# Optimization experiments

Measured on AMD Instinct MI355X. Metric: run time of the kernel, lower is better.

## Reference

```python
import jax, jax.numpy as jnp
import numpy as np

H = 768        # hidden_size (rubert-base)
WDIM = 30      # width_embedding_dim (SpanRepresentation default)
MAXW = 10      # max_span_width
HID = 150      # PairwiseScorer hidden_dim
LN_EPS = 1e-5


def setup_inputs() -> dict:
    key = jax.random.key(0)
    ks = jax.random.split(key, 12)
    B, S, N = 4, 2048, 4096
    p = lambda i, shape: jax.random.normal(ks[i], shape, dtype=jnp.float32) * 0.02
    return {
        "sequence_output": jax.random.normal(ks[0], (B, S, H), dtype=jnp.float32),
        "span_starts": jax.random.randint(ks[1], (B, N), 0, S),
        "span_ends": jax.random.randint(ks[2], (B, N), 0, S),
        "W_start": p(3, (H, H)), "b_start": jnp.zeros((H,), jnp.float32),
        "W_end": p(4, (H, H)), "b_end": jnp.zeros((H,), jnp.float32),
        "width_emb": p(5, (MAXW + 1, WDIM)),
        "W_out": p(6, (2 * H + WDIM, H)), "b_out": jnp.zeros((H,), jnp.float32),
        "w_ment": p(7, (H,)), "b_ment": jnp.zeros((), jnp.float32),
        "W1": p(8, (4 * H, HID)), "b1": jnp.zeros((HID,), jnp.float32),
        "ln_g": jnp.ones((HID,), jnp.float32), "ln_b": jnp.zeros((HID,), jnp.float32),
        "W2": p(9, (HID,)), "b2": jnp.zeros((), jnp.float32),
        "top_k": 128,
    }


def reference(sequence_output, span_starts, span_ends,
              W_start, b_start, W_end, b_end, width_emb, W_out, b_out,
              w_ment, b_ment, W1, b1, ln_g, ln_b, W2, b2, top_k):
    # --- SpanRepresentation: gather endpoints, endpoint FFs, width embedding ---
    st = jnp.take_along_axis(sequence_output, span_starts[..., None], axis=1)  # [B,N,H]
    en = jnp.take_along_axis(sequence_output, span_ends[..., None], axis=1)    # [B,N,H]
    start_e = st @ W_start + b_start
    end_e = en @ W_end + b_end
    widths = jnp.clip(span_ends - span_starts, 0, MAXW)
    we = width_emb[widths]                                                     # [B,N,WDIM]
    span_repr = jnp.concatenate([start_e, end_e, we], axis=-1) @ W_out + b_out # [B,N,H]

    # --- MentionScorer + top-k filtering (per batch, vectorized) ---
    scores = span_repr @ w_ment + b_ment                                       # [B,N]
    mention_scores, idx = jax.lax.top_k(scores, top_k)                         # [B,K]
    repr_k = jnp.take_along_axis(span_repr, idx[..., None], axis=1)            # [B,K,H]
    f_starts = jnp.take_along_axis(span_starts, idx, axis=1)
    f_ends = jnp.take_along_axis(span_ends, idx, axis=1)

    # --- PairwiseScorer over all pairs: cat([s1,s2,s1-s2,s1*s2]) @ W1 ---
    # Split W1 rows into the four feature blocks; fold the (s1-s2) block in:
    #   z = s1@(Wa+Wc) + s2@(Wb-Wc) + (s1*s2)@Wd + b1
    Wa, Wb, Wc, Wd = W1[:H], W1[H:2*H], W1[2*H:3*H], W1[3*H:]
    u = repr_k @ (Wa + Wc)                                                     # [B,K,HID]
    v = repr_k @ (Wb - Wc)                                                     # [B,K,HID]
    pw = jnp.einsum('bih,bjh,hd->bijd', repr_k, repr_k, Wd)                    # [B,K,K,HID]
    z = u[:, :, None, :] + v[:, None, :, :] + pw + b1
    h = jax.nn.relu(z)
    mu = jnp.mean(h, axis=-1, keepdims=True)
    var = jnp.mean(jnp.square(h - mu), axis=-1, keepdims=True)
    hn = (h - mu) * jax.lax.rsqrt(var + LN_EPS) * ln_g + ln_b
    # Dropout(0.3) is identity in eval mode.
    ant = hn @ W2 + b2                                                         # [B,K,K]
    ant = jnp.tril(ant, k=-1)

    return (mention_scores, ant, f_starts, f_ends)
```

## Files before the change

### kernel.cpp

```cpp
#include <hip/hip_runtime.h>
#include <math.h>

#define H 768
#define SEQ 2048
#define NSP 4096
#define HIDD 150
#define TOPK 128
#define NPAD 160

#define OFS_ANT 512
#define OFS_FS 66048
#define OFS_FE 66560

static const size_t OFF_T     = 0ull;
static const size_t OFF_BIASP = 8448ull;
static const size_t OFF_WOV   = 14592ull;
static const size_t OFF_AV    = 16128ull;
static const size_t OFF_CV    = 16896ull;
static const size_t OFF_TW    = 17664ull;
static const size_t OFF_PD    = 17680ull;
static const size_t OFF_CAND  = 34064ull;
static const size_t OFF_FS    = 42256ull;
static const size_t OFF_FE    = 42768ull;
static const size_t OFF_WID   = 43280ull;
static const size_t OFF_UVP   = 43792ull;
static const size_t OFF_GW    = 371472ull;
static const size_t OFF_SCAL  = 371632ull;
static const size_t OFF_WF    = 371640ull;
static const size_t OFF_WCF   = 433080ull;
static const size_t OFF_WSF   = 555960ull;
static const size_t OFF_WEF   = 850872ull;
static const size_t OFF_WOF   = 1145784ull;
static const size_t OFF_SEH   = 1735608ull;
static const size_t OFF_RKH   = 2128824ull;

typedef __attribute__((ext_vector_type(8))) _Float16 half8;
typedef __attribute__((ext_vector_type(4))) _Float16 half4;
typedef __attribute__((ext_vector_type(4))) float f32x4;

__global__ __launch_bounds__(256) void kA(
    const float* __restrict__ b_start, const float* __restrict__ b_end,
    const float* __restrict__ b_out, const float* __restrict__ W_out,
    const float* __restrict__ w_ment, const float* __restrict__ W1,
    const float* __restrict__ ln_g, const float* __restrict__ ln_b,
    const float* __restrict__ W2, const float* __restrict__ b2,
    const float* __restrict__ W_start, const float* __restrict__ W_end,
    float* __restrict__ biasP, float* __restrict__ WOV,
    _Float16* __restrict__ WF, _Float16* __restrict__ WCF,
    _Float16* __restrict__ WSF, _Float16* __restrict__ WEF,
    _Float16* __restrict__ WOF, float* __restrict__ GW, float* __restrict__ SCAL,
    float* __restrict__ ant) {
    const int blk = blockIdx.x, tid = threadIdx.x;
    if (blk < 24) {
        const int kc = blk / 3, jb = blk - kc * 3;
        const int j = jb * 256 + tid;
        float acc = (kc == 0) ? b_out[j] : 0.f;
        const int k0 = kc * 96;
#pragma unroll 4
        for (int k = k0; k < k0 + 96; ++k) {
            acc += b_start[k] * W_out[(size_t)k * H + j];
            acc += b_end[k]   * W_out[(size_t)(H + k) * H + j];
        }
        biasP[kc * H + j] = acc;
    } else if (blk < 408) {
        const int wid = tid >> 6, lane = tid & 63;
        const int gr = (blk - 24) * 4 + wid;
        const float* row = W_out + (size_t)gr * H;
        float s = 0.f;
#pragma unroll
        for (int q = 0; q < 12; ++q) s += row[lane + 64 * q] * w_ment[lane + 64 * q];
#pragma unroll
        for (int off = 32; off; off >>= 1) s += __shfl_down(s, off, 64);
        if (lane == 0) WOV[gr] = s;
    } else if (blk < 468) {
        const int idx = (blk - 408) * 256 + tid;
        const int nt = idx / 1536;
        const int rem = idx - nt * 1536;
        const int kt = rem >> 6, lane = rem & 63;
        const int n = nt * 16 + (lane & 15);
        const int kb = kt * 32 + (lane >> 4) * 8;
        _Float16* dst = WF + ((size_t)((kt * 10 + nt) * 64 + lane)) * 8;
#pragma unroll
        for (int e = 0; e < 8; ++e) {
            float v = (n < HIDD) ? W1[(size_t)(3 * H + kb + e) * HIDD + n] : 0.f;
            dst[e] = (_Float16)v;
        }
    } else if (blk < 588) {
        const int idx = (blk - 468) * 256 + tid;
        const int nt = idx / 1536;
        const int rem = idx - nt * 1536;
        const int kt = rem >> 6, lane = rem & 63;
        const int n = nt * 16 + (lane & 15);
        const int kb = kt * 32 + (lane >> 4) * 8;
        _Float16* dst = WCF + (size_t)idx * 8;
#pragma unroll
        for (int e = 0; e < 8; ++e) {
            const int h = kb + e;
            float v = 0.f;
            if (n < 160) {
                if (n < HIDD)
                    v = W1[(size_t)h * HIDD + n] + W1[(size_t)(2 * H + h) * HIDD + n];
            } else {
                const int d = n - 160;
                if (d < HIDD)
                    v = W1[(size_t)(H + h) * HIDD + d] - W1[(size_t)(2 * H + h) * HIDD + d];
            }
            dst[e] = (_Float16)v;
        }
    } else if (blk == 588) {
        if (tid < NPAD) GW[tid] = (tid < HIDD) ? ln_g[tid] * W2[tid] : 0.f;
        if (tid == 0) {
            float sg = 0.f, sb = 0.f;
            for (int d = 0; d < HIDD; ++d) { sg += ln_g[d] * W2[d]; sb += ln_b[d] * W2[d]; }
            SCAL[0] = sg;
            SCAL[1] = sb + b2[0];
        }
    } else if (blk < 1165) {
        const bool isS = blk < 877;
        const int idx = (blk - (isS ? 589 : 877)) * 256 + tid;
        const float* Wsrc = isS ? W_start : W_end;
        _Float16* dstb = isS ? WSF : WEF;
        const int nt = idx / 1536;
        const int rem = idx - nt * 1536;
        const int kt = rem >> 6, lane = rem & 63;
        const int n = nt * 16 + (lane & 15);
        const int kb = kt * 32 + (lane >> 4) * 8;
        _Float16* dst = dstb + (size_t)idx * 8;
#pragma unroll
        for (int e = 0; e < 8; ++e) dst[e] = (_Float16)Wsrc[(size_t)(kb + e) * H + n];
    } else if (blk < 1741) {
        const int idx = (blk - 1165) * 256 + tid;
        const int nt = idx / 3072;
        const int rem = idx - nt * 3072;
        const int kt = rem >> 6, lane = rem & 63;
        const int n = nt * 16 + (lane & 15);
        const int kb = kt * 32 + (lane >> 4) * 8;
        _Float16* dst = WOF + (size_t)idx * 8;
#pragma unroll
        for (int e = 0; e < 8; ++e) dst[e] = (_Float16)W_out[(size_t)(kb + e) * H + n];
    } else {
        const int idx = (blk - 1741) * 256 + tid;
        *(float4*)(ant + (size_t)idx * 4) = make_float4(0.f, 0.f, 0.f, 0.f);
    }
}

__global__ __launch_bounds__(256) void kB(
    const float* __restrict__ biasP, const float* __restrict__ width_emb,
    const float* __restrict__ W_out, const float* __restrict__ W_start,
    const float* __restrict__ W_end, const float* __restrict__ WOV,
    float* __restrict__ T, float* __restrict__ av, float* __restrict__ cv) {
    const int blk = blockIdx.x, tid = threadIdx.x;
    if (blk < 33) {
        const int w = blk / 3, jb = blk - w * 3;
        const int j = jb * 256 + tid;
        float acc = 0.f;
#pragma unroll
        for (int kc = 0; kc < 8; ++kc) acc += biasP[kc * H + j];
#pragma unroll
        for (int k = 0; k < 30; ++k)
            acc += width_emb[w * 30 + k] * W_out[(size_t)(2 * H + k) * H + j];
        T[w * H + j] = acc;
    } else {
        const int wid = tid >> 6, lane = tid & 63;
        const int gr = (blk - 33) * 4 + wid;
        const float* row = (gr < H) ? (W_start + (size_t)gr * H) : (W_end + (size_t)(gr - H) * H);
        const float* vec = (gr < H) ? WOV : (WOV + H);
        float s = 0.f;
#pragma unroll
        for (int q = 0; q < 12; ++q) s += row[lane + 64 * q] * vec[lane + 64 * q];
#pragma unroll
        for (int off = 32; off; off >>= 1) s += __shfl_down(s, off, 64);
        if (lane == 0) {
            if (gr < H) av[gr] = s; else cv[gr - H] = s;
        }
    }
}

__global__ void k_posdots(const float* __restrict__ seq, const float* __restrict__ av,
                          const float* __restrict__ cv, const float* __restrict__ T,
                          const float* __restrict__ w_ment, const float* __restrict__ b_ment,
                          float* __restrict__ PD, float* __restrict__ tw) {
    const int wid = threadIdx.x >> 6, lane = threadIdx.x & 63;
    if (blockIdx.x < 2048) {
        const int r = blockIdx.x * 4 + wid;
        const float4* row = (const float4*)(seq + (size_t)r * H);
        const float4* a4 = (const float4*)av;
        const float4* c4 = (const float4*)cv;
        float sa = 0.f, sc = 0.f;
#pragma unroll
        for (int q = 0; q < 3; ++q) {
            float4 x = row[lane + 64 * q];
            float4 ya = a4[lane + 64 * q], yc = c4[lane + 64 * q];
            sa += x.x * ya.x + x.y * ya.y + x.z * ya.z + x.w * ya.w;
            sc += x.x * yc.x + x.y * yc.y + x.z * yc.z + x.w * yc.w;
        }
#pragma unroll
        for (int off = 32; off; off >>= 1) {
            sa += __shfl_down(sa, off, 64);
            sc += __shfl_down(sc, off, 64);
        }
        if (lane == 0) { PD[r] = sa; PD[8192 + r] = sc; }
    } else {
        for (int w = wid; w <= 10; w += 4) {
            float s = 0.f;
#pragma unroll
            for (int q = 0; q < 12; ++q) s += T[w * H + lane + 64 * q] * w_ment[lane + 64 * q];
#pragma unroll
            for (int off = 32; off; off >>= 1) s += __shfl_down(s, off, 64);
            if (lane == 0) tw[w] = s + b_ment[0];
        }
    }
}

__global__ __launch_bounds__(256) void k_sort1(const float* __restrict__ PD,
    const int* __restrict__ starts, const int* __restrict__ ends,
    const float* __restrict__ tw, unsigned long long* __restrict__ CAND) {
    __shared__ unsigned long long keys[512];
    const int blk = blockIdx.x;
    const int b = blk >> 3, c = blk & 7;
    const int tid = threadIdx.x;
    for (int i = tid; i < 512; i += 256) {
        const int gi = c * 512 + i;
        const int r = b * NSP + gi;
        const int s = starts[r], e = ends[r];
        int w = e - s; w = w < 0 ? 0 : (w > 10 ? 10 : w);
        const float sc = PD[b * SEQ + s] + PD[8192 + b * SEQ + e] + tw[w];
        unsigned u = __float_as_uint(sc);
        u = (u & 0x80000000u) ? ~u : (u | 0x80000000u);
        keys[i] = ((unsigned long long)u << 32) | (unsigned)(0xFFFFFFFFu - (unsigned)gi);
    }
    __syncthreads();
    for (int k = 2; k <= 512; k <<= 1) {
        for (int j = k >> 1; j > 0; j >>= 1) {
            const int p = tid;
            const int i = ((p & ~(j - 1)) << 1) | (p & (j - 1));
            const int l = i | j;
            unsigned long long a = keys[i], d = keys[l];
            const bool desc = ((i & k) == 0);
            if ((a < d) == desc) { keys[i] = d; keys[l] = a; }
            __syncthreads();
        }
    }
    if (tid < 128) CAND[(size_t)(b * 8 + c) * 128 + tid] = keys[tid];
}

__global__ __launch_bounds__(256) void k_sort2(const unsigned long long* __restrict__ CAND,
    const int* __restrict__ starts, const int* __restrict__ ends,
    float* __restrict__ out, int* __restrict__ fsI, int* __restrict__ feI,
    int* __restrict__ widI) {
    __shared__ unsigned long long K[1024];
    const int b = blockIdx.x, tid = threadIdx.x;
    for (int i = tid; i < 1024; i += 256) K[i] = CAND[(size_t)b * 1024 + i];
    __syncthreads();
    for (int nl = 4; nl >= 1; nl >>= 1) {
        const int items = nl * 128;
        unsigned long long v0 = 0, v1 = 0;
        if (tid < items) {
            const int q = tid >> 7, r = tid & 127;
            unsigned long long a = K[q * 256 + r];
            unsigned long long d = K[q * 256 + 128 + (127 - r)];
            v0 = a > d ? a : d;
        }
        if (tid + 256 < items) {
            const int i = tid + 256;
            const int q = i >> 7, r = i & 127;
            unsigned long long a = K[q * 256 + r];
            unsigned long long d = K[q * 256 + 128 + (127 - r)];
            v1 = a > d ? a : d;
        }
        __syncthreads();
        if (tid < items) K[(tid >> 7) * 128 + (tid & 127)] = v0;
        if (tid + 256 < items) { const int i = tid + 256; K[(i >> 7) * 128 + (i & 127)] = v1; }
        __syncthreads();
        for (int j = 64; j; j >>= 1) {
            const int pairs = nl * 64;
            for (int i = tid; i < pairs; i += 256) {
                const int q = i >> 6, r = i & 63;
                const int lo = q * 128 + (((r & ~(j - 1)) << 1) | (r & (j - 1)));
                const int hi = lo + j;
                unsigned long long a = K[lo], d = K[hi];
                if (a < d) { K[lo] = d; K[hi] = a; }
            }
            __syncthreads();
        }
    }
    if (tid < TOPK) {
        const unsigned long long key = K[tid];
        const int widx = (int)(0xFFFFFFFFu - (unsigned)(key & 0xFFFFFFFFu));
        const unsigned hu = (unsigned)(key >> 32);
        const float sval = __uint_as_float((hu & 0x80000000u) ? (hu & 0x7FFFFFFFu) : ~hu);
        const int s = starts[b * NSP + widx], e = ends[b * NSP + widx];
        const int p = b * TOPK + tid;
        out[p] = sval;
        out[OFS_FS + p] = (float)s;
        out[OFS_FE + p] = (float)e;
        fsI[p] = b * SEQ + s;
        feI[p] = b * SEQ + e;
        int w = e - s;
        widI[p] = w < 0 ? 0 : (w > 10 ? 10 : w);
    }
}

__global__ __launch_bounds__(256) void k_gemm1(const float* __restrict__ seq,
    const int* __restrict__ fsI, const int* __restrict__ feI,
    const _Float16* __restrict__ WSF, const _Float16* __restrict__ WEF,
    _Float16* __restrict__ SEH) {
    const int mt = blockIdx.x;
    const int wave = threadIdx.x >> 6, lane = threadIdx.x & 63;
    const int g = lane >> 4;
    const int nt0 = blockIdx.y * 8 + wave * 2;
    const int gi = mt * 16 + (lane & 15);
    const int src = (mt < 32) ? fsI[gi] : feI[gi - 512];
    const float* Arow = seq + (size_t)src * H + g * 8;
    const _Float16* BF = (mt < 32) ? WSF : WEF;
    f32x4 acc0 = {0.f, 0.f, 0.f, 0.f}, acc1 = acc0;
    for (int kt = 0; kt < 24; ++kt) {
        float4 v0 = *(const float4*)(Arow + kt * 32);
        float4 v1 = *(const float4*)(Arow + kt * 32 + 4);
        half8 a = {(_Float16)v0.x, (_Float16)v0.y, (_Float16)v0.z, (_Float16)v0.w,
                   (_Float16)v1.x, (_Float16)v1.y, (_Float16)v1.z, (_Float16)v1.w};
        half8 b0 = *(const half8*)(BF + ((size_t)((nt0 * 24 + kt) * 64 + lane)) * 8);
        half8 b1 = *(const half8*)(BF + ((size_t)(((nt0 + 1) * 24 + kt) * 64 + lane)) * 8);
        acc0 = __builtin_amdgcn_mfma_f32_16x16x32_f16(a, b0, acc0, 0, 0, 0);
        acc1 = __builtin_amdgcn_mfma_f32_16x16x32_f16(a, b1, acc1, 0, 0, 0);
    }
    const int c = lane & 15, quad = lane >> 4;
#pragma unroll
    for (int r = 0; r < 4; ++r) {
        const int row = mt * 16 + quad * 4 + r;
        SEH[(size_t)row * H + nt0 * 16 + c] = (_Float16)acc0[r];
        SEH[(size_t)row * H + (nt0 + 1) * 16 + c] = (_Float16)acc1[r];
    }
}

__global__ __launch_bounds__(256) void k_gemm2(const _Float16* __restrict__ SEH,
    const _Float16* __restrict__ WOF, const float* __restrict__ T,
    const int* __restrict__ widI, _Float16* __restrict__ RKH) {
    const int mt = blockIdx.x;
    const int wave = threadIdx.x >> 6, lane = threadIdx.x & 63;
    const int nt0 = blockIdx.y * 8 + wave * 2;
    const _Float16* A0 = SEH + (size_t)(mt * 16 + (lane & 15)) * H + (lane >> 4) * 8;
    const _Float16* A1 = SEH + (size_t)(512 + mt * 16 + (lane & 15)) * H + (lane >> 4) * 8;
    f32x4 acc0 = {0.f, 0.f, 0.f, 0.f}, acc1 = acc0;
    for (int kt = 0; kt < 48; ++kt) {
        half8 a = (kt < 24) ? *(const half8*)(A0 + kt * 32)
                            : *(const half8*)(A1 + (kt - 24) * 32);
        half8 b0 = *(const half8*)(WOF + ((size_t)((nt0 * 48 + kt) * 64 + lane)) * 8);
        half8 b1 = *(const half8*)(WOF + ((size_t)(((nt0 + 1) * 48 + kt) * 64 + lane)) * 8);
        acc0 = __builtin_amdgcn_mfma_f32_16x16x32_f16(a, b0, acc0, 0, 0, 0);
        acc1 = __builtin_amdgcn_mfma_f32_16x16x32_f16(a, b1, acc1, 0, 0, 0);
    }
    const int c = lane & 15, quad = lane >> 4;
#pragma unroll
    for (int r = 0; r < 4; ++r) {
        const int row = mt * 16 + quad * 4 + r;
        const float* Tr = T + (size_t)widI[row] * H;
        RKH[(size_t)row * H + nt0 * 16 + c] = (_Float16)(acc0[r] + Tr[nt0 * 16 + c]);
        RKH[(size_t)row * H + (nt0 + 1) * 16 + c] = (_Float16)(acc1[r] + Tr[(nt0 + 1) * 16 + c]);
    }
}

__global__ __launch_bounds__(256) void k_uv3(const _Float16* __restrict__ RKH,
    const _Float16* __restrict__ WCF, float* __restrict__ UVP) {
    const int t = blockIdx.x, kh = blockIdx.y;
    const int wave = threadIdx.x >> 6, lane = threadIdx.x & 63;
    const _Float16* Arow = RKH + (size_t)(t * 16 + (lane & 15)) * H + (lane >> 4) * 8;
    f32x4 acc[5];
#pragma unroll
    for (int q = 0; q < 5; ++q) acc[q] = (f32x4){0.f, 0.f, 0.f, 0.f};
    for (int kk = 0; kk < 12; ++kk) {
        const int kt = kh * 12 + kk;
        half8 a = *(const half8*)(Arow + kt * 32);
#pragma unroll
        for (int q = 0; q < 5; ++q) {
            const int nt = wave * 5 + q;
            half8 bv = *(const half8*)(WCF + ((size_t)((nt * 24 + kt) * 64 + lane)) * 8);
            acc[q] = __builtin_amdgcn_mfma_f32_16x16x32_f16(a, bv, acc[q], 0, 0, 0);
        }
    }
    const int c = lane & 15, g = lane >> 4;
#pragma unroll
    for (int q = 0; q < 5; ++q) {
        const int n = (wave * 5 + q) * 16 + c;
#pragma unroll
        for (int r = 0; r < 4; ++r) {
            const int p = t * 16 + g * 4 + r;
            UVP[((size_t)kh * 512 + p) * 320 + n] = acc[q][r];
        }
    }
}

__global__ __launch_bounds__(256) void k_pair(
    const _Float16* __restrict__ WF, const _Float16* __restrict__ RKH,
    const float* __restrict__ UVP, const float* __restrict__ b1,
    const float* __restrict__ GW, const float* __restrict__ SCAL,
    float* __restrict__ ant) {
    const int b = blockIdx.y;
    int ti = 0, rem = blockIdx.x;
    while (rem >= (ti >> 1) + 1) { rem -= (ti >> 1) + 1; ++ti; }
    const int tj = rem;
    const int wave = threadIdx.x >> 6, lane = threadIdx.x & 63;
    const int g = lane >> 4, c = lane & 15;
    const int i0 = ti * 8 + wave * 2;
    const int j0 = tj * 16;

    const _Float16* Ri0 = RKH + (size_t)(b * TOPK + i0) * H + g * 8;
    const _Float16* Ri1 = RKH + (size_t)(b * TOPK + i0 + 1) * H + g * 8;
    const _Float16* Rj  = RKH + (size_t)(b * TOPK + j0 + c) * H + g * 8;

    f32x4 acc0[10], acc1[10];
#pragma unroll
    for (int nt = 0; nt < 10; ++nt) {
        acc0[nt] = (f32x4){0.f, 0.f, 0.f, 0.f};
        acc1[nt] = (f32x4){0.f, 0.f, 0.f, 0.f};
    }

    for (int kt = 0; kt < 24; ++kt) {
        half8 bv[10];
        const _Float16* wsrc = WF + (size_t)kt * 5120 + (size_t)lane * 8;
#pragma unroll
        for (int nt = 0; nt < 10; ++nt) bv[nt] = *(const half8*)(wsrc + nt * 512);
        half8 rj  = *(const half8*)(Rj + kt * 32);
        half8 ri0 = *(const half8*)(Ri0 + kt * 32);
        half8 ri1 = *(const half8*)(Ri1 + kt * 32);
        half8 a0 = ri0 * rj;
        half8 a1 = ri1 * rj;
#pragma unroll
        for (int nt = 0; nt < 10; ++nt) {
            acc0[nt] = __builtin_amdgcn_mfma_f32_16x16x32_f16(a0, bv[nt], acc0[nt], 0, 0, 0);
            acc1[nt] = __builtin_amdgcn_mfma_f32_16x16x32_f16(a1, bv[nt], acc1[nt], 0, 0, 0);
        }
    }

    const float Sgw = SCAL[0], C0 = SCAL[1];
    float gw10[10];
#pragma unroll
    for (int nt = 0; nt < 10; ++nt) gw10[nt] = GW[nt * 16 + c];

#pragma unroll
    for (int iw = 0; iw < 2; ++iw) {
        const int i = i0 + iw;
        const int pi = b * TOPK + i;
        float u10[10];
#pragma unroll
        for (int nt = 0; nt < 10; ++nt) {
            const int d = nt * 16 + c;
            const float ub = (d < HIDD) ? b1[d] : 0.f;
            u10[nt] = UVP[(size_t)pi * 320 + d] + UVP[(size_t)(512 + pi) * 320 + d] + ub;
        }
        const f32x4* acc = iw ? acc1 : acc0;
#pragma unroll
        for (int r = 0; r < 4; ++r) {
            const int j = j0 + g * 4 + r;
            const int pj = b * TOPK + j;
            const float* Vp0 = UVP + (size_t)pj * 320 + 160;
            const float* Vp1 = UVP + (size_t)(512 + pj) * 320 + 160;
            float s1 = 0.f, s2 = 0.f, s3 = 0.f;
#pragma unroll
            for (int nt = 0; nt < 10; ++nt) {
                const int d = nt * 16 + c;
                float z = acc[nt][r] + u10[nt] + Vp0[d] + Vp1[d];
                float h = (d < HIDD && z > 0.f) ? z : 0.f;
                s1 += h;
                s2 += h * h;
                s3 += h * gw10[nt];
            }
#pragma unroll
            for (int off = 1; off < 16; off <<= 1) {
                s1 += __shfl_xor(s1, off, 64);
                s2 += __shfl_xor(s2, off, 64);
                s3 += __shfl_xor(s3, off, 64);
            }
            const float mu = s1 * (1.f / HIDD);
            const float var = s2 * (1.f / HIDD) - mu * mu;
            const float rstd = rsqrtf(var + 1e-5f);
            const float val = rstd * (s3 - mu * Sgw) + C0;
            if (c == 0 && j < i) ant[((size_t)b * TOPK + i) * TOPK + j] = val;
        }
    }
}

extern "C" void kernel_launch(void* const* d_in, const int* in_sizes, int n_in,
                              void* d_out, int out_size, void* d_ws, size_t ws_size,
                              hipStream_t stream) {
    const float* seq      = (const float*)d_in[0];
    const int*   starts   = (const int*)d_in[1];
    const int*   ends     = (const int*)d_in[2];
    const float* W_start  = (const float*)d_in[3];
    const float* b_start  = (const float*)d_in[4];
    const float* W_end    = (const float*)d_in[5];
    const float* b_end    = (const float*)d_in[6];
    const float* width_e  = (const float*)d_in[7];
    const float* W_out    = (const float*)d_in[8];
    const float* b_out    = (const float*)d_in[9];
    const float* w_ment   = (const float*)d_in[10];
    const float* b_ment   = (const float*)d_in[11];
    const float* W1       = (const float*)d_in[12];
    const float* b1       = (const float*)d_in[13];
    const float* ln_g     = (const float*)d_in[14];
    const float* ln_b     = (const float*)d_in[15];
    const float* W2       = (const float*)d_in[16];
    const float* b2       = (const float*)d_in[17];
    float* out = (float*)d_out;
    float* ws  = (float*)d_ws;

    float* Tt    = ws + OFF_T;
    float* biasP = ws + OFF_BIASP;
    float* WOV   = ws + OFF_WOV;
    float* av    = ws + OFF_AV;
    float* cv    = ws + OFF_CV;
    float* tw    = ws + OFF_TW;
    float* PD    = ws + OFF_PD;
    unsigned long long* CANDp = (unsigned long long*)(ws + OFF_CAND);
    int*   fsI   = (int*)(ws + OFF_FS);
    int*   feI   = (int*)(ws + OFF_FE);
    int*   widI  = (int*)(ws + OFF_WID);
    float* UVPp  = ws + OFF_UVP;
    float* GWp   = ws + OFF_GW;
    float* SCALp = ws + OFF_SCAL;
    _Float16* WFp   = (_Float16*)(ws + OFF_WF);
    _Float16* WCFp  = (_Float16*)(ws + OFF_WCF);
    _Float16* WSFp  = (_Float16*)(ws + OFF_WSF);
    _Float16* WEFp  = (_Float16*)(ws + OFF_WEF);
    _Float16* WOFp  = (_Float16*)(ws + OFF_WOF);
    _Float16* SEHp  = (_Float16*)(ws + OFF_SEH);
    _Float16* RKHp  = (_Float16*)(ws + OFF_RKH);

    kA<<<1805, 256, 0, stream>>>(b_start, b_end, b_out, W_out, w_ment, W1,
                                 ln_g, ln_b, W2, b2, W_start, W_end,
                                 biasP, WOV, WFp, WCFp, WSFp, WEFp, WOFp, GWp, SCALp,
                                 out + OFS_ANT);
    kB<<<417, 256, 0, stream>>>(biasP, width_e, W_out, W_start, W_end, WOV, Tt, av, cv);
    k_posdots<<<2049, 256, 0, stream>>>(seq, av, cv, Tt, w_ment, b_ment, PD, tw);
    k_sort1<<<32, 256, 0, stream>>>(PD, starts, ends, tw, CANDp);
    k_sort2<<<4, 256, 0, stream>>>(CANDp, starts, ends, out, fsI, feI, widI);
    k_gemm1<<<dim3(64, 6), 256, 0, stream>>>(seq, fsI, feI, WSFp, WEFp, SEHp);
    k_gemm2<<<dim3(32, 6), 256, 0, stream>>>(SEHp, WOFp, Tt, widI, RKHp);
    k_uv3<<<dim3(32, 2), 256, 0, stream>>>(RKHp, WCFp, UVPp);
    k_pair<<<dim3(72, 4), 256, 0, stream>>>(WFp, RKHp, UVPp, b1, GWp, SCALp,
                                            out + OFS_ANT);
}
```

Before: 228.4 us.

## Prefetch next K-slice in GEMM kernels and split-K the output projection

```diff
diff --git a/kernel.cpp b/kernel.cpp
--- a/kernel.cpp
+++ b/kernel.cpp
@@ -33,6 +33,7 @@
 static const size_t OFF_WOF   = 1145784ull;
 static const size_t OFF_SEH   = 1735608ull;
 static const size_t OFF_RKH   = 2128824ull;
+static const size_t OFF_RKP2  = 2325432ull;
 
 typedef __attribute__((ext_vector_type(8))) _Float16 half8;
 typedef __attribute__((ext_vector_type(4))) _Float16 half4;
@@ -314,15 +315,24 @@
     const float* Arow = seq + (size_t)src * H + g * 8;
     const _Float16* BF = (mt < 32) ? WSF : WEF;
     f32x4 acc0 = {0.f, 0.f, 0.f, 0.f}, acc1 = acc0;
+    float4 v0 = *(const float4*)(Arow);
+    float4 v1 = *(const float4*)(Arow + 4);
+    half8 b0 = *(const half8*)(BF + ((size_t)(nt0 * 24) * 64 + lane) * 8);
+    half8 b1 = *(const half8*)(BF + ((size_t)((nt0 + 1) * 24) * 64 + lane) * 8);
     for (int kt = 0; kt < 24; ++kt) {
-        float4 v0 = *(const float4*)(Arow + kt * 32);
-        float4 v1 = *(const float4*)(Arow + kt * 32 + 4);
+        float4 nv0, nv1;
+        half8 nb0, nb1;
+        if (kt < 23) {
+            nv0 = *(const float4*)(Arow + (kt + 1) * 32);
+            nv1 = *(const float4*)(Arow + (kt + 1) * 32 + 4);
+            nb0 = *(const half8*)(BF + ((size_t)(nt0 * 24 + kt + 1) * 64 + lane) * 8);
+            nb1 = *(const half8*)(BF + ((size_t)((nt0 + 1) * 24 + kt + 1) * 64 + lane) * 8);
+        }
         half8 a = {(_Float16)v0.x, (_Float16)v0.y, (_Float16)v0.z, (_Float16)v0.w,
                    (_Float16)v1.x, (_Float16)v1.y, (_Float16)v1.z, (_Float16)v1.w};
-        half8 b0 = *(const half8*)(BF + ((size_t)((nt0 * 24 + kt) * 64 + lane)) * 8);
-        half8 b1 = *(const half8*)(BF + ((size_t)(((nt0 + 1) * 24 + kt) * 64 + lane)) * 8);
         acc0 = __builtin_amdgcn_mfma_f32_16x16x32_f16(a, b0, acc0, 0, 0, 0);
         acc1 = __builtin_amdgcn_mfma_f32_16x16x32_f16(a, b1, acc1, 0, 0, 0);
+        if (kt < 23) { v0 = nv0; v1 = nv1; b0 = nb0; b1 = nb1; }
     }
     const int c = lane & 15, quad = lane >> 4;
 #pragma unroll
@@ -334,48 +344,81 @@
 }
 
 __global__ __launch_bounds__(256) void k_gemm2(const _Float16* __restrict__ SEH,
-    const _Float16* __restrict__ WOF, const float* __restrict__ T,
-    const int* __restrict__ widI, _Float16* __restrict__ RKH) {
-    const int mt = blockIdx.x;
+    const _Float16* __restrict__ WOF, float* __restrict__ RKP2) {
+    const int mt = blockIdx.x, kh = blockIdx.z;
     const int wave = threadIdx.x >> 6, lane = threadIdx.x & 63;
     const int nt0 = blockIdx.y * 8 + wave * 2;
-    const _Float16* A0 = SEH + (size_t)(mt * 16 + (lane & 15)) * H + (lane >> 4) * 8;
-    const _Float16* A1 = SEH + (size_t)(512 + mt * 16 + (lane & 15)) * H + (lane >> 4) * 8;
+    const _Float16* Arow = SEH + (size_t)(kh * 512 + mt * 16 + (lane & 15)) * H + (lane >> 4) * 8;
+    const _Float16* B0 = WOF + ((size_t)(nt0 * 48 + kh * 24) * 64 + lane) * 8;
+    const _Float16* B1 = WOF + ((size_t)((nt0 + 1) * 48 + kh * 24) * 64 + lane) * 8;
     f32x4 acc0 = {0.f, 0.f, 0.f, 0.f}, acc1 = acc0;
-    for (int kt = 0; kt < 48; ++kt) {
-        half8 a = (kt < 24) ? *(const half8*)(A0 + kt * 32)
-                            : *(const half8*)(A1 + (kt - 24) * 32);
-        half8 b0 = *(const half8*)(WOF + ((size_t)((nt0 * 48 + kt) * 64 + lane)) * 8);
-        half8 b1 = *(const half8*)(WOF + ((size_t)(((nt0 + 1) * 48 + kt) * 64 + lane)) * 8);
+    half8 a = *(const half8*)(Arow);
+    half8 b0 = *(const half8*)(B0);
+    half8 b1 = *(const half8*)(B1);
+    for (int kt2 = 0; kt2 < 24; ++kt2) {
+        half8 na, nb0, nb1;
+        if (kt2 < 23) {
+            na = *(const half8*)(Arow + (kt2 + 1) * 32);
+            nb0 = *(const half8*)(B0 + (size_t)(kt2 + 1) * 512);
+            nb1 = *(const half8*)(B1 + (size_t)(kt2 + 1) * 512);
+        }
         acc0 = __builtin_amdgcn_mfma_f32_16x16x32_f16(a, b0, acc0, 0, 0, 0);
         acc1 = __builtin_amdgcn_mfma_f32_16x16x32_f16(a, b1, acc1, 0, 0, 0);
+        if (kt2 < 23) { a = na; b0 = nb0; b1 = nb1; }
     }
     const int c = lane & 15, quad = lane >> 4;
+    float* dst = RKP2 + (size_t)kh * 512 * H;
 #pragma unroll
     for (int r = 0; r < 4; ++r) {
         const int row = mt * 16 + quad * 4 + r;
-        const float* Tr = T + (size_t)widI[row] * H;
-        RKH[(size_t)row * H + nt0 * 16 + c] = (_Float16)(acc0[r] + Tr[nt0 * 16 + c]);
-        RKH[(size_t)row * H + (nt0 + 1) * 16 + c] = (_Float16)(acc1[r] + Tr[(nt0 + 1) * 16 + c]);
-    }
+        dst[(size_t)row * H + nt0 * 16 + c] = acc0[r];
+        dst[(size_t)row * H + (nt0 + 1) * 16 + c] = acc1[r];
+    }
+}
+
+__global__ void k_fin(const float* __restrict__ RKP2, const float* __restrict__ T,
+                      const int* __restrict__ widI, _Float16* __restrict__ RKH) {
+    const int p = blockIdx.x, tid = threadIdx.x;
+    if (tid >= 192) return;
+    const int w = widI[p];
+    const int c0 = tid * 4;
+    float4 s = *(const float4*)(T + (size_t)w * H + c0);
+    float4 v0 = *(const float4*)(RKP2 + (size_t)p * H + c0);
+    float4 v1 = *(const float4*)(RKP2 + (size_t)(512 + p) * H + c0);
+    half4 h = {(_Float16)(s.x + v0.x + v1.x), (_Float16)(s.y + v0.y + v1.y),
+               (_Float16)(s.z + v0.z + v1.z), (_Float16)(s.w + v0.w + v1.w)};
+    *(half4*)(RKH + (size_t)p * H + c0) = h;
 }
 
 __global__ __launch_bounds__(256) void k_uv3(const _Float16* __restrict__ RKH,
     const _Float16* __restrict__ WCF, float* __restrict__ UVP) {
     const int t = blockIdx.x, kh = blockIdx.y;
     const int wave = threadIdx.x >> 6, lane = threadIdx.x & 63;
-    const _Float16* Arow = RKH + (size_t)(t * 16 + (lane & 15)) * H + (lane >> 4) * 8;
+    const _Float16* Arow = RKH + (size_t)(t * 16 + (lane & 15)) * H + (lane >> 4) * 8 + kh * 384;
     f32x4 acc[5];
 #pragma unroll
     for (int q = 0; q < 5; ++q) acc[q] = (f32x4){0.f, 0.f, 0.f, 0.f};
+    half8 a = *(const half8*)(Arow);
+    half8 bv[5], nbv[5];
+#pragma unroll
+    for (int q = 0; q < 5; ++q)
+        bv[q] = *(const half8*)(WCF + ((size_t)(((wave * 5 + q) * 24 + kh * 12) * 64 + lane)) * 8);
     for (int kk = 0; kk < 12; ++kk) {
-        const int kt = kh * 12 + kk;
-        half8 a = *(const half8*)(Arow + kt * 32);
-#pragma unroll
-        for (int q = 0; q < 5; ++q) {
-            const int nt = wave * 5 + q;
-            half8 bv = *(const half8*)(WCF + ((size_t)((nt * 24 + kt) * 64 + lane)) * 8);
-            acc[q] = __builtin_amdgcn_mfma_f32_16x16x32_f16(a, bv, acc[q], 0, 0, 0);
+        half8 na;
+        if (kk < 11) {
+            const int kt = kh * 12 + kk + 1;
+            na = *(const half8*)(Arow + (kk + 1) * 32);
+#pragma unroll
+            for (int q = 0; q < 5; ++q)
+                nbv[q] = *(const half8*)(WCF + ((size_t)(((wave * 5 + q) * 24 + kt) * 64 + lane)) * 8);
+        }
+#pragma unroll
+        for (int q = 0; q < 5; ++q)
+            acc[q] = __builtin_amdgcn_mfma_f32_16x16x32_f16(a, bv[q], acc[q], 0, 0, 0);
+        if (kk < 11) {
+            a = na;
+#pragma unroll
+            for (int q = 0; q < 5; ++q) bv[q] = nbv[q];
         }
     }
     const int c = lane & 15, g = lane >> 4;
@@ -390,7 +433,7 @@
     }
 }
 
-__global__ __launch_bounds__(256) void k_pair(
+__global__ __launch_bounds__(256, 1) void k_pair(
     const _Float16* __restrict__ WF, const _Float16* __restrict__ RKH,
     const float* __restrict__ UVP, const float* __restrict__ b1,
     const float* __restrict__ GW, const float* __restrict__ SCAL,
@@ -407,6 +450,7 @@
     const _Float16* Ri0 = RKH + (size_t)(b * TOPK + i0) * H + g * 8;
     const _Float16* Ri1 = RKH + (size_t)(b * TOPK + i0 + 1) * H + g * 8;
     const _Float16* Rj  = RKH + (size_t)(b * TOPK + j0 + c) * H + g * 8;
+    const _Float16* Wl  = WF + (size_t)lane * 8;
 
     f32x4 acc0[10], acc1[10];
 #pragma unroll
@@ -415,20 +459,34 @@
         acc1[nt] = (f32x4){0.f, 0.f, 0.f, 0.f};
     }
 
+    half8 bv[10], nbv[10];
+    half8 rj, ri0, ri1, nrj, nri0, nri1;
+#pragma unroll
+    for (int nt = 0; nt < 10; ++nt) bv[nt] = *(const half8*)(Wl + (size_t)nt * 512);
+    rj  = *(const half8*)(Rj);
+    ri0 = *(const half8*)(Ri0);
+    ri1 = *(const half8*)(Ri1);
+
     for (int kt = 0; kt < 24; ++kt) {
-        half8 bv[10];
-        const _Float16* wsrc = WF + (size_t)kt * 5120 + (size_t)lane * 8;
-#pragma unroll
-        for (int nt = 0; nt < 10; ++nt) bv[nt] = *(const half8*)(wsrc + nt * 512);
-        half8 rj  = *(const half8*)(Rj + kt * 32);
-        half8 ri0 = *(const half8*)(Ri0 + kt * 32);
-        half8 ri1 = *(const half8*)(Ri1 + kt * 32);
+        if (kt < 23) {
+            const _Float16* wsrc = Wl + (size_t)(kt + 1) * 5120;
+#pragma unroll
+            for (int nt = 0; nt < 10; ++nt) nbv[nt] = *(const half8*)(wsrc + (size_t)nt * 512);
+            nrj  = *(const half8*)(Rj + (kt + 1) * 32);
+            nri0 = *(const half8*)(Ri0 + (kt + 1) * 32);
+            nri1 = *(const half8*)(Ri1 + (kt + 1) * 32);
+        }
         half8 a0 = ri0 * rj;
         half8 a1 = ri1 * rj;
 #pragma unroll
         for (int nt = 0; nt < 10; ++nt) {
             acc0[nt] = __builtin_amdgcn_mfma_f32_16x16x32_f16(a0, bv[nt], acc0[nt], 0, 0, 0);
             acc1[nt] = __builtin_amdgcn_mfma_f32_16x16x32_f16(a1, bv[nt], acc1[nt], 0, 0, 0);
+        }
+        if (kt < 23) {
+#pragma unroll
+            for (int nt = 0; nt < 10; ++nt) bv[nt] = nbv[nt];
+            rj = nrj; ri0 = nri0; ri1 = nri1;
         }
     }
 
@@ -525,6 +583,7 @@
     _Float16* WOFp  = (_Float16*)(ws + OFF_WOF);
     _Float16* SEHp  = (_Float16*)(ws + OFF_SEH);
     _Float16* RKHp  = (_Float16*)(ws + OFF_RKH);
+    float* RKP2p = ws + OFF_RKP2;
 
     kA<<<1805, 256, 0, stream>>>(b_start, b_end, b_out, W_out, w_ment, W1,
                                  ln_g, ln_b, W2, b2, W_start, W_end,
@@ -535,7 +594,8 @@
     k_sort1<<<32, 256, 0, stream>>>(PD, starts, ends, tw, CANDp);
     k_sort2<<<4, 256, 0, stream>>>(CANDp, starts, ends, out, fsI, feI, widI);
     k_gemm1<<<dim3(64, 6), 256, 0, stream>>>(seq, fsI, feI, WSFp, WEFp, SEHp);
-    k_gemm2<<<dim3(32, 6), 256, 0, stream>>>(SEHp, WOFp, Tt, widI, RKHp);
+    k_gemm2<<<dim3(32, 6, 2), 256, 0, stream>>>(SEHp, WOFp, RKP2p);
+    k_fin<<<512, 192, 0, stream>>>(RKP2p, Tt, widI, RKHp);
     k_uv3<<<dim3(32, 2), 256, 0, stream>>>(RKHp, WCFp, UVPp);
     k_pair<<<dim3(72, 4), 256, 0, stream>>>(WFp, RKHp, UVPp, b1, GWp, SCALp,
                                             out + OFS_ANT);
```

Result: faster. 201.8 us (-11.7%).
